# Kernel optimization log

Hardware: AMD Instinct MI355X
Metric: run time of the kernel (lower is better)

The kernel has to match this reference:

```python
import jax, jax.numpy as jnp
import numpy as np

N = 8192
VOCAB = 50000
EDIM = 256
WFEAT = 256
SLOPE = 0.01
NEG_INF = -1e9


def _gat_layer(x, adj, W, a_src, a_dst):
    # x: [N, Fin], adj: [N, N] (binary, self-loops included)
    h = x @ W                                   # [N, Fout]
    s = h @ a_src                               # [N] attention source term
    d = h @ a_dst                               # [N] attention dest term
    e = jax.nn.leaky_relu(s[:, None] + d[None, :], negative_slope=SLOPE)  # [N, N]
    e = jnp.where(adj > 0, e, NEG_INF)
    attn = jax.nn.softmax(e, axis=1)            # per-node softmax over neighbors
    out = attn @ h                              # scatter-aggregate
    return out, attn


def setup_inputs() -> dict:
    key = jax.random.key(0)
    ks = jax.random.split(key, 10)
    inDoc = jax.random.randint(ks[0], (N,), 0, VOCAB)
    p = 32.0 / N  # avg degree ~32
    eye = jnp.eye(N, dtype=jnp.float32)
    adj0 = jnp.clip(jax.random.bernoulli(ks[1], p, (N, N)).astype(jnp.float32) + eye, 0.0, 1.0)
    adj1 = jnp.clip(jax.random.bernoulli(ks[2], p, (N, N)).astype(jnp.float32) + eye, 0.0, 1.0)
    sc_e = 1.0 / np.sqrt(EDIM)
    sc_w = 1.0 / np.sqrt(WFEAT)
    emb = jax.random.normal(ks[3], (VOCAB, EDIM), dtype=jnp.float32) * sc_e
    W1 = jax.random.normal(ks[4], (EDIM, WFEAT), dtype=jnp.float32) * sc_e
    a1_src = jax.random.normal(ks[5], (WFEAT,), dtype=jnp.float32) * sc_w
    a1_dst = jax.random.normal(ks[6], (WFEAT,), dtype=jnp.float32) * sc_w
    W2 = jax.random.normal(ks[7], (WFEAT, WFEAT), dtype=jnp.float32) * sc_w
    a2_src = jax.random.normal(ks[8], (WFEAT,), dtype=jnp.float32) * sc_w
    a2_dst = jax.random.normal(ks[9], (WFEAT,), dtype=jnp.float32) * sc_w
    return {"inDoc": inDoc, "adj0": adj0, "adj1": adj1, "emb": emb,
            "W1": W1, "a1_src": a1_src, "a1_dst": a1_dst,
            "W2": W2, "a2_src": a2_src, "a2_dst": a2_dst}


def reference(inDoc, adj0, adj1, emb, W1, a1_src, a1_dst, W2, a2_src, a2_dst):
    words = emb[inDoc]                              # embedding lookup [N, EDIM]
    words, sattention = _gat_layer(words, adj0, W1, a1_src, a1_dst)
    document, dattention = _gat_layer(words, adj1, W2, a2_src, a2_dst)
    document = document + words                     # residual
    docMean = jnp.mean(document, axis=0)            # [WFEAT]
    return docMean, sattention, dattention
```

## Files before the change

kernel.cpp:

```cpp
#include <hip/hip_runtime.h>
#include <cstddef>

#define NN 8192
#define FD 256
#define LSLOPE 0.01f
#define NEGF -3.0e38f
#define CAP 192

typedef float f4 __attribute__((ext_vector_type(4)));

__global__ __launch_bounds__(256) void gemm_sd_kernel(
    const float* __restrict__ X,
    const int*   __restrict__ idx,
    const float* __restrict__ emb,
    const float* __restrict__ W,
    const float* __restrict__ a_src,
    const float* __restrict__ a_dst,
    float*       __restrict__ H,
    float*       __restrict__ s,
    float*       __restrict__ d)
{
    __shared__ __align__(16) float xs[16][FD];
    __shared__ __align__(16) f4    wbuf[2048];
    const int tid = threadIdx.x;
    const int n0  = blockIdx.x * 16;

    #pragma unroll
    for (int r = 0; r < 16; ++r) {
        const float* src = idx ? (emb + (size_t)idx[n0 + r] * FD)
                               : (X + (size_t)(n0 + r) * FD);
        xs[r][tid] = src[tid];
    }

    const int wave = tid >> 6;
    const int lane = tid & 63;
    const int c0 = lane * 4;
    const int r0 = wave * 4;
    const f4* W4 = reinterpret_cast<const f4*>(W);

    float acc[4][4] = {};
    for (int st = 0; st < FD / 32; ++st) {
        #pragma unroll
        for (int p = 0; p < 8; ++p)
            wbuf[p * 256 + tid] = W4[st * 2048 + p * 256 + tid];
        __syncthreads();

        #pragma unroll 4
        for (int kk = 0; kk < 32; ++kk) {
            const int k = st * 32 + kk;
            f4 w = wbuf[kk * 64 + lane];
            #pragma unroll
            for (int r = 0; r < 4; ++r) {
                float x = xs[r0 + r][k];
                acc[r][0] = fmaf(x, w[0], acc[r][0]);
                acc[r][1] = fmaf(x, w[1], acc[r][1]);
                acc[r][2] = fmaf(x, w[2], acc[r][2]);
                acc[r][3] = fmaf(x, w[3], acc[r][3]);
            }
        }
        __syncthreads();
    }

    const float4 as4 = *reinterpret_cast<const float4*>(a_src + c0);
    const float4 ad4 = *reinterpret_cast<const float4*>(a_dst + c0);

    #pragma unroll
    for (int r = 0; r < 4; ++r) {
        float4 o = make_float4(acc[r][0], acc[r][1], acc[r][2], acc[r][3]);
        *reinterpret_cast<float4*>(H + (size_t)(n0 + r0 + r) * FD + c0) = o;

        float ps = acc[r][0]*as4.x + acc[r][1]*as4.y + acc[r][2]*as4.z + acc[r][3]*as4.w;
        float pd = acc[r][0]*ad4.x + acc[r][1]*ad4.y + acc[r][2]*ad4.z + acc[r][3]*ad4.w;
        #pragma unroll
        for (int off = 32; off > 0; off >>= 1) {
            ps += __shfl_xor(ps, off);
            pd += __shfl_xor(pd, off);
        }
        if (lane == 0) {
            s[n0 + r0 + r] = ps;
            d[n0 + r0 + r] = pd;
        }
    }
}

__global__ __launch_bounds__(256, 6) void attn_kernel(
    const float* __restrict__ adj,
    const float* __restrict__ svec,
    const float* __restrict__ dvec,
    const float* __restrict__ H,
    const float* residual,
    float* __restrict__ attn_out,
    float* out_rows)
{
    __shared__ int   jbuf_s[4 * CAP];
    __shared__ float pbuf_s[4 * CAP];

    const int tid  = threadIdx.x;
    const int lane = tid & 63;
    const int wv   = tid >> 6;
    const int i    = blockIdx.x * 4 + wv;

    int*   jbuf = jbuf_s + wv * CAP;
    float* pbuf = pbuf_s + wv * CAP;

    f4* orow4 = reinterpret_cast<f4*>(attn_out + (size_t)i * NN);
    const f4 z = {0.f, 0.f, 0.f, 0.f};
    #pragma unroll
    for (int q = 0; q < 32; ++q)
        __builtin_nontemporal_store(z, &orow4[q * 64 + lane]);

    const f4* arow4 = reinterpret_cast<const f4*>(adj + (size_t)i * NN);
    const unsigned long long lt = (lane == 0) ? 0ull : (~0ull >> (64 - lane));
    int base = 0;
    #pragma unroll
    for (int c = 0; c < 8; ++c) {
        f4 av[4];
        #pragma unroll
        for (int k = 0; k < 4; ++k)
            av[k] = __builtin_nontemporal_load(&arow4[c * 256 + k * 64 + lane]);
        #pragma unroll
        for (int k = 0; k < 4; ++k) {
            #pragma unroll
            for (int q = 0; q < 4; ++q) {
                const bool nz = (av[k][q] != 0.f);
                const unsigned long long mask = __ballot(nz);
                if (nz) {
                    const int pos = base + (int)__popcll(mask & lt);
                    if (pos < CAP)
                        jbuf[pos] = (c * 1024) + (k * 256) + (lane * 4) + q;
                }
                base += (int)__popcll(mask);
            }
        }
    }
    const int nnz = (base < CAP) ? base : CAP;

    const float si = svec[i];
    float mloc = NEGF;
    for (int t = lane; t < nnz; t += 64) {
        float e = si + dvec[jbuf[t]];
        e = (e >= 0.f) ? e : LSLOPE * e;
        pbuf[t] = e;
        mloc = fmaxf(mloc, e);
    }
    #pragma unroll
    for (int off = 32; off > 0; off >>= 1) mloc = fmaxf(mloc, __shfl_xor(mloc, off));
    const float m = mloc;

    float sloc = 0.f;
    for (int t = lane; t < nnz; t += 64) {
        float p = __expf(pbuf[t] - m);
        pbuf[t] = p;
        sloc += p;
    }
    #pragma unroll
    for (int off = 32; off > 0; off >>= 1) sloc += __shfl_xor(sloc, off);
    const float inv = 1.f / sloc;

    asm volatile("s_waitcnt vmcnt(0)" ::: "memory");
    for (int t = lane; t < nnz; t += 64) {
        float pn = pbuf[t] * inv;
        pbuf[t] = pn;
        attn_out[(size_t)i * NN + jbuf[t]] = pn;
    }

    const f4* H4 = reinterpret_cast<const f4*>(H);
    f4 a0 = {0.f, 0.f, 0.f, 0.f};
    f4 a1 = {0.f, 0.f, 0.f, 0.f};
    int t = 0;
    for (; t + 2 <= nnz; t += 2) {
        const float p0 = pbuf[t];     const int j0 = jbuf[t];
        const float p1 = pbuf[t + 1]; const int j1 = jbuf[t + 1];
        a0 += p0 * H4[(size_t)j0 * 64 + lane];
        a1 += p1 * H4[(size_t)j1 * 64 + lane];
    }
    if (t < nnz)
        a0 += pbuf[t] * H4[(size_t)jbuf[t] * 64 + lane];
    f4 o = a0 + a1;
    if (residual)
        o += reinterpret_cast<const f4*>(residual)[(size_t)i * 64 + lane];
    reinterpret_cast<f4*>(out_rows)[(size_t)i * 64 + lane] = o;
}

__global__ __launch_bounds__(256) void colsum_partial(
    const float* __restrict__ doc, float* __restrict__ partial)
{
    const int tid = threadIdx.x;
    const int b = blockIdx.x;
    float acc = 0.f;
    const float* p = doc + (size_t)b * 64 * FD + tid;
    #pragma unroll 8
    for (int r = 0; r < 64; ++r) acc += p[(size_t)r * FD];
    partial[b * FD + tid] = acc;
}

__global__ __launch_bounds__(256) void colsum_final(
    const float* __restrict__ partial, float* __restrict__ out)
{
    const int tid = threadIdx.x;
    float acc = 0.f;
    for (int b = 0; b < 128; ++b) acc += partial[b * FD + tid];
    out[tid] = acc * (1.f / (float)NN);
}

extern "C" void kernel_launch(void* const* d_in, const int* in_sizes, int n_in,
                              void* d_out, int out_size, void* d_ws, size_t ws_size,
                              hipStream_t stream)
{
    const int*   inDoc = (const int*)d_in[0];
    const float* adj0  = (const float*)d_in[1];
    const float* adj1  = (const float*)d_in[2];
    const float* emb   = (const float*)d_in[3];
    const float* W1    = (const float*)d_in[4];
    const float* a1s   = (const float*)d_in[5];
    const float* a1d   = (const float*)d_in[6];
    const float* W2    = (const float*)d_in[7];
    const float* a2s   = (const float*)d_in[8];
    const float* a2d   = (const float*)d_in[9];

    float* out     = (float*)d_out;
    float* docMean = out;
    float* sattn   = out + 256;
    float* dattn   = out + 256 + (size_t)NN * NN;

    float* ws = (float*)d_ws;
    float* h   = ws;
    float* o1  = ws + (size_t)NN * FD;
    float* s1  = ws + 2 * (size_t)NN * FD;
    float* d1  = s1 + NN;
    float* s2  = d1 + NN;
    float* d2  = s2 + NN;
    float* partial = d2 + NN;

    gemm_sd_kernel<<<NN / 16, 256, 0, stream>>>(nullptr, inDoc, emb, W1, a1s, a1d, h, s1, d1);
    attn_kernel<<<NN / 4, 256, 0, stream>>>(adj0, s1, d1, h, nullptr, sattn, o1);

    gemm_sd_kernel<<<NN / 16, 256, 0, stream>>>(o1, nullptr, nullptr, W2, a2s, a2d, h, s2, d2);
    attn_kernel<<<NN / 4, 256, 0, stream>>>(adj1, s2, d2, h, o1, dattn, o1);

    colsum_partial<<<128, 256, 0, stream>>>(o1, partial);
    colsum_final<<<1, 256, 0, stream>>>(partial, docMean);
}
```

Baseline: 294.0 us.

## Write attention rows once with dense stores instead of zero-fill plus scatter

Each lane keeps a per-lane bitmask of adjacency hits. A wave-level prefix scan of per-lane counts replaces the per-element ballots used for compaction. The attention row is then written in a single pass of dense nontemporal f4 stores that carry the normalized values in place, instead of zero-filling the row and then doing scattered scalar writes after a vmcnt wait. Normalization is deferred to the aggregation output by multiplying by inv once. The risk is extra register use for the masks and longer serial ctz loops per lane.

```diff
diff --git a/kernel.cpp b/kernel.cpp
--- a/kernel.cpp
+++ b/kernel.cpp
@@ -103,15 +103,9 @@
     int*   jbuf = jbuf_s + wv * CAP;
     float* pbuf = pbuf_s + wv * CAP;
 
-    f4* orow4 = reinterpret_cast<f4*>(attn_out + (size_t)i * NN);
-    const f4 z = {0.f, 0.f, 0.f, 0.f};
-    #pragma unroll
-    for (int q = 0; q < 32; ++q)
-        __builtin_nontemporal_store(z, &orow4[q * 64 + lane]);
-
     const f4* arow4 = reinterpret_cast<const f4*>(adj + (size_t)i * NN);
-    const unsigned long long lt = (lane == 0) ? 0ull : (~0ull >> (64 - lane));
-    int base = 0;
+    unsigned int mask[4] = {0u, 0u, 0u, 0u};
+    int cnt = 0;
     #pragma unroll
     for (int c = 0; c < 8; ++c) {
         f4 av[4];
@@ -122,18 +116,39 @@
         for (int k = 0; k < 4; ++k) {
             #pragma unroll
             for (int q = 0; q < 4; ++q) {
-                const bool nz = (av[k][q] != 0.f);
-                const unsigned long long mask = __ballot(nz);
-                if (nz) {
-                    const int pos = base + (int)__popcll(mask & lt);
-                    if (pos < CAP)
-                        jbuf[pos] = (c * 1024) + (k * 256) + (lane * 4) + q;
-                }
-                base += (int)__popcll(mask);
-            }
-        }
-    }
-    const int nnz = (base < CAP) ? base : CAP;
+                const unsigned int nz = (av[k][q] != 0.f) ? 1u : 0u;
+                cnt += (int)nz;
+                mask[c >> 1] |= nz << (((c & 1) << 4) | (k << 2) | q);
+            }
+        }
+    }
+
+    int x = cnt;
+    #pragma unroll
+    for (int off = 1; off < 64; off <<= 1) {
+        int y = __shfl_up(x, off);
+        if (lane >= off) x += y;
+    }
+    const int lane_start = x - cnt;
+    const int total = __shfl(x, 63);
+    const int nnz = (total < CAP) ? total : CAP;
+
+    {
+        int pos = lane_start;
+        #pragma unroll
+        for (int w = 0; w < 4; ++w) {
+            unsigned int mw = mask[w];
+            while (mw) {
+                const int b = __builtin_ctz(mw);
+                mw &= mw - 1;
+                const int n = (w << 5) | b;
+                const int j = ((n >> 4) << 10) | (((n >> 2) & 3) << 8)
+                            | (lane << 2) | (n & 3);
+                if (pos < CAP) jbuf[pos] = j;
+                ++pos;
+            }
+        }
+    }
 
     const float si = svec[i];
     float mloc = NEGF;
@@ -157,11 +172,28 @@
     for (int off = 32; off > 0; off >>= 1) sloc += __shfl_xor(sloc, off);
     const float inv = 1.f / sloc;
 
-    asm volatile("s_waitcnt vmcnt(0)" ::: "memory");
-    for (int t = lane; t < nnz; t += 64) {
-        float pn = pbuf[t] * inv;
-        pbuf[t] = pn;
-        attn_out[(size_t)i * NN + jbuf[t]] = pn;
+    f4* orow4 = reinterpret_cast<f4*>(attn_out + (size_t)i * NN);
+    {
+        int pos = lane_start;
+        #pragma unroll
+        for (int w = 0; w < 4; ++w) {
+            const unsigned int mw = mask[w];
+            #pragma unroll
+            for (int g = 0; g < 8; ++g) {
+                f4 o = {0.f, 0.f, 0.f, 0.f};
+                const unsigned int bits = (mw >> (g * 4)) & 0xFu;
+                #pragma unroll
+                for (int q = 0; q < 4; ++q) {
+                    if (bits & (1u << q)) {
+                        if (pos < CAP) o[q] = pbuf[pos] * inv;
+                        ++pos;
+                    }
+                }
+                const int n0 = (w << 5) | (g << 2);
+                const int slot = ((n0 >> 4) << 8) | (((n0 >> 2) & 3) << 6) | lane;
+                __builtin_nontemporal_store(o, &orow4[slot]);
+            }
+        }
     }
 
     const f4* H4 = reinterpret_cast<const f4*>(H);
@@ -176,7 +208,7 @@
     }
     if (t < nnz)
         a0 += pbuf[t] * H4[(size_t)jbuf[t] * 64 + lane];
-    f4 o = a0 + a1;
+    f4 o = (a0 + a1) * inv;
     if (residual)
         o += reinterpret_cast<const f4*>(residual)[(size_t)i * 64 + lane];
     reinterpret_cast<f4*>(out_rows)[(size_t)i * 64 + lane] = o;
```

Measured after the change: 324.9 us. 1.11x slower.
